# Kernel optimization log

Measured on AMD Instinct MI355X. Metric: run time of the kernel, lower is better.

## Reference

```python
import jax, jax.numpy as jnp
import numpy as np

B, S, D, H = 2, 2048, 1024, 16
DK = D // H


def setup_inputs() -> dict:
    key = jax.random.key(0)
    ks = jax.random.split(key, 12)
    sc = 1.0 / np.sqrt(D)
    inp = {
        'q': jax.random.normal(ks[0], (B, S, D), jnp.float32),
        'k': jax.random.normal(ks[1], (B, S, D), jnp.float32),
        'v': jax.random.normal(ks[2], (B, S, D), jnp.float32),
        'mask': jnp.tril(jnp.ones((S, S), jnp.int32))[None, None],  # causal [1,1,S,S]
        'w_q': jax.random.normal(ks[3], (D, D), jnp.float32) * sc,
        'b_q': jnp.zeros((D,), jnp.float32),
        'w_k': jax.random.normal(ks[4], (D, D), jnp.float32) * sc,
        'b_k': jnp.zeros((D,), jnp.float32),
        'w_v': jax.random.normal(ks[5], (D, D), jnp.float32) * sc,
        'b_v': jnp.zeros((D,), jnp.float32),
        'w_o': jax.random.normal(ks[6], (D, D), jnp.float32) * sc,
        'b_o': jnp.zeros((D,), jnp.float32),
    }
    return inp


def _split_heads(x):
    # [B,S,D] -> [B,H,S,DK]
    b, s, _ = x.shape
    return x.reshape(b, s, H, DK).transpose(0, 2, 1, 3)


def reference(q, k, v, mask, w_q, b_q, w_k, b_k, w_v, b_v, w_o, b_o):
    # Linear projections (torch Linear: x @ W.T + b)
    qh = _split_heads(q @ w_q.T + b_q)
    kh = _split_heads(k @ w_k.T + b_k)
    vh = _split_heads(v @ w_v.T + b_v)
    scores = jnp.einsum('bhqd,bhkd->bhqk', qh, kh) / jnp.sqrt(jnp.float32(DK))
    scores = jnp.where(mask == 0, jnp.float32(-1e9), scores)
    probs = jax.nn.softmax(scores, axis=-1)
    # dropout is identity in eval mode
    ctx = jnp.einsum('bhqk,bhkd->bhqd', probs, vh)  # [B,H,S,DK]
    ctx = ctx.transpose(0, 2, 1, 3).reshape(q.shape[0], -1, D)
    out = ctx @ w_o.T + b_o
    return out, probs
```

## Files before the change

kernel.cpp:

```cpp
#include <hip/hip_runtime.h>

typedef float f32x4 __attribute__((ext_vector_type(4)));
typedef short s16x8 __attribute__((ext_vector_type(8)));
typedef short s16x4 __attribute__((ext_vector_type(4)));

#define MFMA(a, b, c) __builtin_amdgcn_mfma_f32_16x16x32_bf16((a), (b), (c), 0, 0, 0)

static __device__ __forceinline__ short f2bf(float f) {
  union { float ff; unsigned u; } v; v.ff = f;
  unsigned r = v.u + 0x7FFFu + ((v.u >> 16) & 1u);
  return (short)(r >> 16);
}
static __device__ __forceinline__ float bf2f(short s) {
  union { unsigned u; float f; } v;
  v.u = ((unsigned)(unsigned short)s) << 16;
  return v.f;
}

typedef __attribute__((address_space(3))) void lds_void_t;
typedef const __attribute__((address_space(1))) void gmem_void_t;
static __device__ __forceinline__ void gload_lds16(const void* g, void* l) {
  __builtin_amdgcn_global_load_lds((gmem_void_t*)g, (lds_void_t*)l, 16, 0, 0);
}

__global__ __launch_bounds__(256) void cvt_qkv_kernel(
    const float* __restrict__ q, const float* __restrict__ k, const float* __restrict__ v,
    short* __restrict__ qo, short* __restrict__ ko, short* __restrict__ vo) {
  const int y = blockIdx.y;
  const float* s = (y == 0) ? q : (y == 1) ? k : v;
  short* d = (y == 0) ? qo : (y == 1) ? ko : vo;
  const int i = blockIdx.x * 256 + threadIdx.x;
  const f32x4* s4 = (const f32x4*)s;
  f32x4 a = s4[2 * i], b = s4[2 * i + 1];
  s16x8 o;
  o[0] = f2bf(a[0]); o[1] = f2bf(a[1]); o[2] = f2bf(a[2]); o[3] = f2bf(a[3]);
  o[4] = f2bf(b[0]); o[5] = f2bf(b[1]); o[6] = f2bf(b[2]); o[7] = f2bf(b[3]);
  ((s16x8*)d)[i] = o;
}

__global__ __launch_bounds__(256) void cvt_w_kernel(
    const float* __restrict__ w0, const float* __restrict__ w1,
    const float* __restrict__ w2, const float* __restrict__ w3,
    short* __restrict__ o0, short* __restrict__ o1,
    short* __restrict__ o2, short* __restrict__ o3) {
  const int y = blockIdx.y;
  const float* s = (y == 0) ? w0 : (y == 1) ? w1 : (y == 2) ? w2 : w3;
  short* d = (y == 0) ? o0 : (y == 1) ? o1 : (y == 2) ? o2 : o3;
  const int i = blockIdx.x * 256 + threadIdx.x;
  const f32x4* s4 = (const f32x4*)s;
  f32x4 a = s4[2 * i], b = s4[2 * i + 1];
  s16x8 o;
  o[0] = f2bf(a[0]); o[1] = f2bf(a[1]); o[2] = f2bf(a[2]); o[3] = f2bf(a[3]);
  o[4] = f2bf(b[0]); o[5] = f2bf(b[1]); o[6] = f2bf(b[2]); o[7] = f2bf(b[3]);
  ((s16x8*)d)[i] = o;
}

template <int MODE, int NFRAG>
static __device__ __forceinline__ void gemm_body(
    const short* __restrict__ A, const short* __restrict__ Bt,
    const float* __restrict__ bias, void* __restrict__ outp) {
  constexpr int BN = NFRAG * 32;
  __shared__ short As[4096];
  __shared__ short Bs[BN * 32];
  const int t = threadIdx.x;
  const int lane = t & 63, wave = t >> 6;
  const int wr = wave >> 1, wc = wave & 1;
  const int lr = lane & 15, lg = lane >> 4;
  const int mBase = blockIdx.x * 128, nBase = blockIdx.y * BN;

  const int rowA = t >> 2, kcA = (t & 3) << 3;
  const short* gA = A + (size_t)(mBase + rowA) * 1024 + kcA;
  const short* gB = Bt + (size_t)(nBase + rowA) * 1024 + kcA;

  f32x4 acc[4][NFRAG] = {};

  for (int k0 = 0; k0 < 1024; k0 += 32) {
    __syncthreads();
    gload_lds16(gA + k0, &As[t * 8]);
    gload_lds16(gA + 64 * 1024 + k0, &As[2048 + t * 8]);
    gload_lds16(gB + k0, &Bs[t * 8]);
    if constexpr (NFRAG == 4) gload_lds16(gB + 64 * 1024 + k0, &Bs[2048 + t * 8]);
    __syncthreads();
    const s16x8* Av = (const s16x8*)As;
    const s16x8* Bv = (const s16x8*)Bs;
    s16x8 af[4], bfr[NFRAG];
#pragma unroll
    for (int m = 0; m < 4; ++m) af[m] = Av[(wr * 64 + m * 16 + lr) * 4 + lg];
#pragma unroll
    for (int n = 0; n < NFRAG; ++n) bfr[n] = Bv[(wc * NFRAG * 16 + n * 16 + lr) * 4 + lg];
#pragma unroll
    for (int m = 0; m < 4; ++m)
#pragma unroll
      for (int n = 0; n < NFRAG; ++n)
        acc[m][n] = MFMA(af[m], bfr[n], acc[m][n]);
  }

  const int row0 = mBase + wr * 64 + lg * 4;
  const int col0 = nBase + wc * NFRAG * 16 + lr;
#pragma unroll
  for (int n = 0; n < NFRAG; ++n) {
    const int col = col0 + n * 16;
    const float bv = bias[col];
#pragma unroll
    for (int m = 0; m < 4; ++m) {
#pragma unroll
      for (int j = 0; j < 4; ++j) {
        const int r = row0 + m * 16 + j;
        const float val = acc[m][n][j] + bv;
        if (MODE == 0) {
          short* o = (short*)outp;
          const int bb = r >> 11, ss = r & 2047, hh = col >> 6, dd = col & 63;
          o[((size_t)(bb * 16 + hh) * 2048 + ss) * 64 + dd] = f2bf(val);
        } else {
          ((float*)outp)[(size_t)r * 1024 + col] = val;
        }
      }
    }
  }
}

__global__ __launch_bounds__(256) void gemm_qkv_kernel(
    const short* __restrict__ qb, const short* __restrict__ kb, const short* __restrict__ vb,
    const short* __restrict__ wqb, const short* __restrict__ wkb, const short* __restrict__ wvb,
    const float* __restrict__ bq, const float* __restrict__ bk, const float* __restrict__ bv,
    short* __restrict__ Qh, short* __restrict__ Kh, short* __restrict__ Vh) {
  const int z = blockIdx.z;
  const short* A  = (z == 0) ? qb : (z == 1) ? kb : vb;
  const short* Bt = (z == 0) ? wqb : (z == 1) ? wkb : wvb;
  const float* bias = (z == 0) ? bq : (z == 1) ? bk : bv;
  short* out = (z == 0) ? Qh : (z == 1) ? Kh : Vh;
  gemm_body<0, 4>(A, Bt, bias, out);
}

__global__ __launch_bounds__(256) void gemm_o_kernel(
    const short* __restrict__ A, const short* __restrict__ Bt,
    const float* __restrict__ bias, float* __restrict__ outp) {
  gemm_body<1, 2>(A, Bt, bias, outp);
}

__global__ __launch_bounds__(256) void attn_kernel(
    const short* __restrict__ Qh, const short* __restrict__ Kh,
    const short* __restrict__ Vh, float* __restrict__ probs,
    short* __restrict__ ctxo) {
  __shared__ short Ks[2][4096];
  __shared__ short Vt[2][4096];
  __shared__ short Pl[4096];
  const int t = threadIdx.x;
  const int lane = t & 63, w = t >> 6;
  const int lr = lane & 15, lg = lane >> 4;
  const int qblk = 31 - blockIdx.x;
  const int bh = blockIdx.y;
  const size_t hb = (size_t)bh * (2048 * 64);
  const int qBase = qblk * 64;

  const short* Kg = Kh + hb;
  const short* Vg = Vh + hb;

  const int qg = qBase + w * 16 + lr;
  const s16x8 qf0 = *(const s16x8*)(Qh + hb + (size_t)qg * 64 + lg * 8);
  const s16x8 qf1 = *(const s16x8*)(Qh + hb + (size_t)qg * 64 + 32 + lg * 8);

  const int x = lr & 7;
  const int px = (lr & 7) << 3;

  {
    const f32x4 zz = {0.f, 0.f, 0.f, 0.f};
#pragma unroll 1
    for (int r = 0; r < 16; ++r) {
      float* prow = probs + (size_t)(bh * 2048 + qBase + w * 16 + r) * 2048;
      for (int c = qBase + 64 + lane * 4; c < 2048; c += 256)
        *(f32x4*)&prow[c] = zz;
    }
  }

  auto stageK = [&](int buf, int kt) {
    const int kBase = kt * 64;
    int c = t, key = c >> 3, slot = c & 7;
    gload_lds16(Kg + (size_t)(kBase + key) * 64 + ((slot ^ (key & 7)) << 3), &Ks[buf][c * 8]);
    c = t + 256; key = c >> 3; slot = c & 7;
    gload_lds16(Kg + (size_t)(kBase + key) * 64 + ((slot ^ (key & 7)) << 3), &Ks[buf][c * 8]);
  };

  float rs = 0.f;
  stageK(0, 0);
  __syncthreads();
  for (int kt = 0; kt <= qblk; ++kt) {
    const int cur = kt & 1;
    if (kt < qblk) stageK(cur ^ 1, kt + 1);
    const s16x8* Kv = (const s16x8*)Ks[cur];
#pragma unroll
    for (int sub = 0; sub < 4; ++sub) {
      const int key = sub * 16 + lr;
      s16x8 kf0 = Kv[key * 8 + (lg ^ x)];
      s16x8 kf1 = Kv[key * 8 + ((lg + 4) ^ x)];
      f32x4 z = {0.f, 0.f, 0.f, 0.f};
      f32x4 sa = MFMA(kf0, qf0, z);
      sa = MFMA(kf1, qf1, sa);
      if (kt < qblk) {
#pragma unroll
        for (int j = 0; j < 4; ++j) rs += __expf(sa[j] * 0.125f);
      } else {
        const int key0 = kt * 64 + sub * 16 + lg * 4;
#pragma unroll
        for (int j = 0; j < 4; ++j)
          if (key0 + j <= qg) rs += __expf(sa[j] * 0.125f);
      }
    }
    __syncthreads();
  }
  rs += __shfl_xor(rs, 16);
  rs += __shfl_xor(rs, 32);
  const float rinv = 1.f / rs;

  const int vkey = lane, vdkb = w * 16;
  auto loadV = [&](int kt, s16x8& v0, s16x8& v1) {
    const s16x8* vsrc = (const s16x8*)(Vg + (size_t)(kt * 64 + vkey) * 64 + vdkb);
    v0 = vsrc[0]; v1 = vsrc[1];
  };
  auto writeV = [&](int buf, const s16x8& v0, const s16x8& v1) {
#pragma unroll
    for (int i = 0; i < 8; ++i) {
      const int r0 = vdkb + i, r1 = vdkb + 8 + i;
      Vt[buf][r0 * 64 + (vkey ^ ((r0 & 7) << 3))] = v0[i];
      Vt[buf][r1 * 64 + (vkey ^ ((r1 & 7) << 3))] = v1[i];
    }
  };

  f32x4 cacc[4] = {};
  {
    s16x8 v0, v1;
    stageK(0, 0);
    loadV(0, v0, v1);
    writeV(0, v0, v1);
    __syncthreads();
  }
  for (int kt = 0; kt <= qblk; ++kt) {
    const int cur = kt & 1;
    const bool pf = (kt < qblk);
    const int kBase = kt * 64;
    s16x8 nv0, nv1;
    if (pf) { stageK(cur ^ 1, kt + 1); loadV(kt + 1, nv0, nv1); }
    const s16x8* Kv = (const s16x8*)Ks[cur];
#pragma unroll
    for (int sub = 0; sub < 4; ++sub) {
      const int key = sub * 16 + lr;
      s16x8 kf0 = Kv[key * 8 + (lg ^ x)];
      s16x8 kf1 = Kv[key * 8 + ((lg + 4) ^ x)];
      f32x4 z = {0.f, 0.f, 0.f, 0.f};
      f32x4 sa = MFMA(kf0, qf0, z);
      sa = MFMA(kf1, qf1, sa);
      const int key0 = kBase + sub * 16 + lg * 4;
      f32x4 p4;
      if (kt < qblk) {
#pragma unroll
        for (int j = 0; j < 4; ++j) p4[j] = __expf(sa[j] * 0.125f) * rinv;
      } else {
#pragma unroll
        for (int j = 0; j < 4; ++j)
          p4[j] = (key0 + j <= qg) ? __expf(sa[j] * 0.125f) * rinv : 0.f;
      }
      s16x4 pb;
      pb[0] = f2bf(p4[0]); pb[1] = f2bf(p4[1]);
      pb[2] = f2bf(p4[2]); pb[3] = f2bf(p4[3]);
      *(s16x4*)&Pl[w * 1024 + lr * 64 + ((sub * 16 + lg * 4) ^ px)] = pb;
    }
#pragma unroll
    for (int it = 0; it < 4; ++it) {
      const int row = it * 4 + lg;
      const int c = lr * 4;
      const s16x4 pb4 = *(const s16x4*)&Pl[w * 1024 + row * 64 + (c ^ ((row & 7) << 3))];
      f32x4 pf4;
      pf4[0] = bf2f(pb4[0]); pf4[1] = bf2f(pb4[1]);
      pf4[2] = bf2f(pb4[2]); pf4[3] = bf2f(pb4[3]);
      *(f32x4*)&probs[(size_t)(bh * 2048 + qBase + w * 16 + row) * 2048 + kBase + c] = pf4;
    }
    if (pf) writeV(cur ^ 1, nv0, nv1);
    const s16x8* Vv = (const s16x8*)Vt[cur];
    const s16x8 pfa = *(const s16x8*)&Pl[w * 1024 + lr * 64 + ((lg * 8) ^ px)];
    const s16x8 pfb = *(const s16x8*)&Pl[w * 1024 + lr * 64 + ((32 + lg * 8) ^ px)];
#pragma unroll
    for (int n = 0; n < 4; ++n) {
      const int row = n * 16 + lr;
      s16x8 vf0 = Vv[row * 8 + (lg ^ x)];
      s16x8 vf1 = Vv[row * 8 + ((lg + 4) ^ x)];
      cacc[n] = MFMA(pfa, vf0, cacc[n]);
      cacc[n] = MFMA(pfb, vf1, cacc[n]);
    }
    __syncthreads();
  }

  const int bb = bh >> 4, hh = bh & 15;
#pragma unroll
  for (int n = 0; n < 4; ++n) {
    const int dcol = hh * 64 + n * 16 + lr;
#pragma unroll
    for (int j = 0; j < 4; ++j) {
      const int srow = qBase + w * 16 + lg * 4 + j;
      ctxo[(size_t)(bb * 2048 + srow) * 1024 + dcol] = f2bf(cacc[n][j]);
    }
  }
}

extern "C" void kernel_launch(void* const* d_in, const int* in_sizes, int n_in,
                              void* d_out, int out_size, void* d_ws, size_t ws_size,
                              hipStream_t stream) {
  const float* q  = (const float*)d_in[0];
  const float* k  = (const float*)d_in[1];
  const float* v  = (const float*)d_in[2];
  const float* wq = (const float*)d_in[4];
  const float* bq = (const float*)d_in[5];
  const float* wk = (const float*)d_in[6];
  const float* bk = (const float*)d_in[7];
  const float* wv = (const float*)d_in[8];
  const float* bv = (const float*)d_in[9];
  const float* wo = (const float*)d_in[10];
  const float* bo = (const float*)d_in[11];

  char* ws = (char*)d_ws;
  const size_t MB = 1u << 20;
  short* qb  = (short*)(ws);
  short* kb  = (short*)(ws + 8 * MB);
  short* vb  = (short*)(ws + 16 * MB);
  short* wqb = (short*)(ws + 24 * MB);
  short* wkb = (short*)(ws + 26 * MB);
  short* wvb = (short*)(ws + 28 * MB);
  short* wob = (short*)(ws + 30 * MB);
  short* Qh  = (short*)(ws + 32 * MB);
  short* Kh  = (short*)(ws + 40 * MB);
  short* Vh  = (short*)(ws + 48 * MB);
  short* ctx = (short*)(ws + 56 * MB);

  float* outp  = (float*)d_out;
  float* probs = outp + (size_t)4096 * 1024;

  cvt_qkv_kernel<<<dim3(2048, 3), 256, 0, stream>>>(q, k, v, qb, kb, vb);
  cvt_w_kernel<<<dim3(512, 4), 256, 0, stream>>>(wq, wk, wv, wo, wqb, wkb, wvb, wob);

  gemm_qkv_kernel<<<dim3(32, 8, 3), 256, 0, stream>>>(
      qb, kb, vb, wqb, wkb, wvb, bq, bk, bv, Qh, Kh, Vh);

  attn_kernel<<<dim3(32, 32), 256, 0, stream>>>(Qh, Kh, Vh, probs, ctx);

  gemm_o_kernel<<<dim3(32, 16), 256, 0, stream>>>(ctx, wob, bo, outp);
}
```

Measured before the change: 750.4 us.

## Split softmax row-sum pass into separate kernel and read K directly from global

Moves the first attention pass, which computes softmax denominators, into its own rowsum_kernel that writes reciprocal row sums to workspace (reusing the qb region, which is dead by then). The attention kernel reads those values instead of recomputing them. Both kernels now load K fragments straight from global memory instead of staging them through double-buffered LDS with async copies. This drops LDS use and barriers and may raise occupancy, at the cost of an extra launch and uncoalesced, repeated global K reads that rely on cache.

Result: slower. 914.8 us (+21.9%).

```diff
diff --git a/kernel.cpp b/kernel.cpp
--- a/kernel.cpp
+++ b/kernel.cpp
@@ -138,11 +138,53 @@
   gemm_body<1, 2>(A, Bt, bias, outp);
 }
 
+__global__ __launch_bounds__(256) void rowsum_kernel(
+    const short* __restrict__ Qh, const short* __restrict__ Kh,
+    float* __restrict__ rinv) {
+  const int t = threadIdx.x;
+  const int lane = t & 63, w = t >> 6;
+  const int lr = lane & 15, lg = lane >> 4;
+  const int qblk = 31 - blockIdx.x;
+  const int bh = blockIdx.y;
+  const size_t hb = (size_t)bh * (2048 * 64);
+  const int qBase = qblk * 64;
+  const int qg = qBase + w * 16 + lr;
+
+  const s16x8 qf0 = *(const s16x8*)(Qh + hb + (size_t)qg * 64 + lg * 8);
+  const s16x8 qf1 = *(const s16x8*)(Qh + hb + (size_t)qg * 64 + 32 + lg * 8);
+  const short* Kg = Kh + hb;
+
+  float rs = 0.f;
+  for (int kt = 0; kt <= qblk; ++kt) {
+    const int kBase = kt * 64;
+#pragma unroll
+    for (int sub = 0; sub < 4; ++sub) {
+      const int key = kBase + sub * 16 + lr;
+      const s16x8 kf0 = *(const s16x8*)(Kg + (size_t)key * 64 + lg * 8);
+      const s16x8 kf1 = *(const s16x8*)(Kg + (size_t)key * 64 + 32 + lg * 8);
+      f32x4 z = {0.f, 0.f, 0.f, 0.f};
+      f32x4 sa = MFMA(kf0, qf0, z);
+      sa = MFMA(kf1, qf1, sa);
+      if (kt < qblk) {
+#pragma unroll
+        for (int j = 0; j < 4; ++j) rs += __expf(sa[j] * 0.125f);
+      } else {
+        const int key0 = kBase + sub * 16 + lg * 4;
+#pragma unroll
+        for (int j = 0; j < 4; ++j)
+          if (key0 + j <= qg) rs += __expf(sa[j] * 0.125f);
+      }
+    }
+  }
+  rs += __shfl_xor(rs, 16);
+  rs += __shfl_xor(rs, 32);
+  if (lg == 0) rinv[bh * 2048 + qg] = 1.f / rs;
+}
+
 __global__ __launch_bounds__(256) void attn_kernel(
     const short* __restrict__ Qh, const short* __restrict__ Kh,
-    const short* __restrict__ Vh, float* __restrict__ probs,
-    short* __restrict__ ctxo) {
-  __shared__ short Ks[2][4096];
+    const short* __restrict__ Vh, const float* __restrict__ rinv_g,
+    float* __restrict__ probs, short* __restrict__ ctxo) {
   __shared__ short Vt[2][4096];
   __shared__ short Pl[4096];
   const int t = threadIdx.x;
@@ -159,6 +201,7 @@
   const int qg = qBase + w * 16 + lr;
   const s16x8 qf0 = *(const s16x8*)(Qh + hb + (size_t)qg * 64 + lg * 8);
   const s16x8 qf1 = *(const s16x8*)(Qh + hb + (size_t)qg * 64 + 32 + lg * 8);
+  const float rinv = rinv_g[bh * 2048 + qg];
 
   const int x = lr & 7;
   const int px = (lr & 7) << 3;
@@ -173,45 +216,6 @@
     }
   }
 
-  auto stageK = [&](int buf, int kt) {
-    const int kBase = kt * 64;
-    int c = t, key = c >> 3, slot = c & 7;
-    gload_lds16(Kg + (size_t)(kBase + key) * 64 + ((slot ^ (key & 7)) << 3), &Ks[buf][c * 8]);
-    c = t + 256; key = c >> 3; slot = c & 7;
-    gload_lds16(Kg + (size_t)(kBase + key) * 64 + ((slot ^ (key & 7)) << 3), &Ks[buf][c * 8]);
-  };
-
-  float rs = 0.f;
-  stageK(0, 0);
-  __syncthreads();
-  for (int kt = 0; kt <= qblk; ++kt) {
-    const int cur = kt & 1;
-    if (kt < qblk) stageK(cur ^ 1, kt + 1);
-    const s16x8* Kv = (const s16x8*)Ks[cur];
-#pragma unroll
-    for (int sub = 0; sub < 4; ++sub) {
-      const int key = sub * 16 + lr;
-      s16x8 kf0 = Kv[key * 8 + (lg ^ x)];
-      s16x8 kf1 = Kv[key * 8 + ((lg + 4) ^ x)];
-      f32x4 z = {0.f, 0.f, 0.f, 0.f};
-      f32x4 sa = MFMA(kf0, qf0, z);
-      sa = MFMA(kf1, qf1, sa);
-      if (kt < qblk) {
-#pragma unroll
-        for (int j = 0; j < 4; ++j) rs += __expf(sa[j] * 0.125f);
-      } else {
-        const int key0 = kt * 64 + sub * 16 + lg * 4;
-#pragma unroll
-        for (int j = 0; j < 4; ++j)
-          if (key0 + j <= qg) rs += __expf(sa[j] * 0.125f);
-      }
-    }
-    __syncthreads();
-  }
-  rs += __shfl_xor(rs, 16);
-  rs += __shfl_xor(rs, 32);
-  const float rinv = 1.f / rs;
-
   const int vkey = lane, vdkb = w * 16;
   auto loadV = [&](int kt, s16x8& v0, s16x8& v1) {
     const s16x8* vsrc = (const s16x8*)(Vg + (size_t)(kt * 64 + vkey) * 64 + vdkb);
@@ -229,7 +233,6 @@
   f32x4 cacc[4] = {};
   {
     s16x8 v0, v1;
-    stageK(0, 0);
     loadV(0, v0, v1);
     writeV(0, v0, v1);
     __syncthreads();
@@ -239,13 +242,12 @@
     const bool pf = (kt < qblk);
     const int kBase = kt * 64;
     s16x8 nv0, nv1;
-    if (pf) { stageK(cur ^ 1, kt + 1); loadV(kt + 1, nv0, nv1); }
-    const s16x8* Kv = (const s16x8*)Ks[cur];
+    if (pf) loadV(kt + 1, nv0, nv1);
 #pragma unroll
     for (int sub = 0; sub < 4; ++sub) {
-      const int key = sub * 16 + lr;
-      s16x8 kf0 = Kv[key * 8 + (lg ^ x)];
-      s16x8 kf1 = Kv[key * 8 + ((lg + 4) ^ x)];
+      const int key = kBase + sub * 16 + lr;
+      const s16x8 kf0 = *(const s16x8*)(Kg + (size_t)key * 64 + lg * 8);
+      const s16x8 kf1 = *(const s16x8*)(Kg + (size_t)key * 64 + 32 + lg * 8);
       f32x4 z = {0.f, 0.f, 0.f, 0.f};
       f32x4 sa = MFMA(kf0, qf0, z);
       sa = MFMA(kf1, qf1, sa);
@@ -329,6 +331,7 @@
   short* Kh  = (short*)(ws + 40 * MB);
   short* Vh  = (short*)(ws + 48 * MB);
   short* ctx = (short*)(ws + 56 * MB);
+  float* rinv = (float*)(ws);
 
   float* outp  = (float*)d_out;
   float* probs = outp + (size_t)4096 * 1024;
@@ -339,7 +342,9 @@
   gemm_qkv_kernel<<<dim3(32, 8, 3), 256, 0, stream>>>(
       qb, kb, vb, wqb, wkb, wvb, bq, bk, bv, Qh, Kh, Vh);
 
-  attn_kernel<<<dim3(32, 32), 256, 0, stream>>>(Qh, Kh, Vh, probs, ctx);
+  rowsum_kernel<<<dim3(32, 32), 256, 0, stream>>>(Qh, Kh, rinv);
+
+  attn_kernel<<<dim3(32, 32), 256, 0, stream>>>(Qh, Kh, Vh, rinv, probs, ctx);
 
   gemm_o_kernel<<<dim3(32, 16), 256, 0, stream>>>(ctx, wob, bo, outp);
 }
```

## Pre-transpose V in a separate kernel and load V fragments directly from global

Applied to the files above, without the earlier changes.

Adds a kernel that writes V transposed per head into workspace, so the attention kernel can load MFMA B-operand fragments for P·V straight from global memory. This drops the LDS double buffer for V and its scalar transposing writes, which cuts LDS use, and launch_bounds now asks for 4 blocks per multiprocessor. In exchange it adds an extra kernel launch and a global round trip for V. The V loads now sit on the critical path each iteration instead of being prefetched into LDS. An unused pointer argument is added to the attention kernel.

Result: slower. 811.5 us (+8.2%).

```diff
diff --git a/kernel.cpp b/kernel.cpp
--- a/kernel.cpp
+++ b/kernel.cpp
@@ -138,12 +138,30 @@
   gemm_body<1, 2>(A, Bt, bias, outp);
 }
 
-__global__ __launch_bounds__(256) void attn_kernel(
+__global__ __launch_bounds__(256) void vtrans_kernel(
+    const short* __restrict__ Vh, short* __restrict__ Vt_g) {
+  const int kBase = blockIdx.x * 64;
+  const int bh = blockIdx.y;
+  const size_t ib = (size_t)bh * (2048 * 64);
+  const size_t ob = (size_t)bh * (64 * 2048);
+  const int t = threadIdx.x;
+  const int dk = t >> 2, k8 = t & 3;
+#pragma unroll
+  for (int h = 0; h < 2; ++h) {
+    const int kk = (k8 + 4 * h) * 8;
+    s16x8 v;
+#pragma unroll
+    for (int j = 0; j < 8; ++j)
+      v[j] = Vh[ib + (size_t)(kBase + kk + j) * 64 + dk];
+    *(s16x8*)&Vt_g[ob + (size_t)dk * 2048 + kBase + kk] = v;
+  }
+}
+
+__global__ __launch_bounds__(256, 4) void attn_kernel(
     const short* __restrict__ Qh, const short* __restrict__ Kh,
-    const short* __restrict__ Vh, float* __restrict__ probs,
-    short* __restrict__ ctxo) {
+    const short* __restrict__ Vt_g, const float* __restrict__ rinv_unused,
+    float* __restrict__ probs, short* __restrict__ ctxo) {
   __shared__ short Ks[2][4096];
-  __shared__ short Vt[2][4096];
   __shared__ short Pl[4096];
   const int t = threadIdx.x;
   const int lane = t & 63, w = t >> 6;
@@ -154,7 +172,7 @@
   const int qBase = qblk * 64;
 
   const short* Kg = Kh + hb;
-  const short* Vg = Vh + hb;
+  const short* Vth = Vt_g + (size_t)bh * (64 * 2048);
 
   const int qg = qBase + w * 16 + lr;
   const s16x8 qf0 = *(const s16x8*)(Qh + hb + (size_t)qg * 64 + lg * 8);
@@ -212,34 +230,13 @@
   rs += __shfl_xor(rs, 32);
   const float rinv = 1.f / rs;
 
-  const int vkey = lane, vdkb = w * 16;
-  auto loadV = [&](int kt, s16x8& v0, s16x8& v1) {
-    const s16x8* vsrc = (const s16x8*)(Vg + (size_t)(kt * 64 + vkey) * 64 + vdkb);
-    v0 = vsrc[0]; v1 = vsrc[1];
-  };
-  auto writeV = [&](int buf, const s16x8& v0, const s16x8& v1) {
-#pragma unroll
-    for (int i = 0; i < 8; ++i) {
-      const int r0 = vdkb + i, r1 = vdkb + 8 + i;
-      Vt[buf][r0 * 64 + (vkey ^ ((r0 & 7) << 3))] = v0[i];
-      Vt[buf][r1 * 64 + (vkey ^ ((r1 & 7) << 3))] = v1[i];
-    }
-  };
-
   f32x4 cacc[4] = {};
-  {
-    s16x8 v0, v1;
-    stageK(0, 0);
-    loadV(0, v0, v1);
-    writeV(0, v0, v1);
-    __syncthreads();
-  }
+  stageK(0, 0);
+  __syncthreads();
   for (int kt = 0; kt <= qblk; ++kt) {
     const int cur = kt & 1;
-    const bool pf = (kt < qblk);
     const int kBase = kt * 64;
-    s16x8 nv0, nv1;
-    if (pf) { stageK(cur ^ 1, kt + 1); loadV(kt + 1, nv0, nv1); }
+    if (kt < qblk) stageK(cur ^ 1, kt + 1);
     const s16x8* Kv = (const s16x8*)Ks[cur];
 #pragma unroll
     for (int sub = 0; sub < 4; ++sub) {
@@ -264,6 +261,13 @@
       pb[2] = f2bf(p4[2]); pb[3] = f2bf(p4[3]);
       *(s16x4*)&Pl[w * 1024 + lr * 64 + ((sub * 16 + lg * 4) ^ px)] = pb;
     }
+    s16x8 vf0[4], vf1[4];
+#pragma unroll
+    for (int n = 0; n < 4; ++n) {
+      const short* vrow = Vth + (size_t)(n * 16 + lr) * 2048 + kBase + lg * 8;
+      vf0[n] = *(const s16x8*)vrow;
+      vf1[n] = *(const s16x8*)(vrow + 32);
+    }
 #pragma unroll
     for (int it = 0; it < 4; ++it) {
       const int row = it * 4 + lg;
@@ -274,17 +278,12 @@
       pf4[2] = bf2f(pb4[2]); pf4[3] = bf2f(pb4[3]);
       *(f32x4*)&probs[(size_t)(bh * 2048 + qBase + w * 16 + row) * 2048 + kBase + c] = pf4;
     }
-    if (pf) writeV(cur ^ 1, nv0, nv1);
-    const s16x8* Vv = (const s16x8*)Vt[cur];
     const s16x8 pfa = *(const s16x8*)&Pl[w * 1024 + lr * 64 + ((lg * 8) ^ px)];
     const s16x8 pfb = *(const s16x8*)&Pl[w * 1024 + lr * 64 + ((32 + lg * 8) ^ px)];
 #pragma unroll
     for (int n = 0; n < 4; ++n) {
-      const int row = n * 16 + lr;
-      s16x8 vf0 = Vv[row * 8 + (lg ^ x)];
-      s16x8 vf1 = Vv[row * 8 + ((lg + 4) ^ x)];
-      cacc[n] = MFMA(pfa, vf0, cacc[n]);
-      cacc[n] = MFMA(pfb, vf1, cacc[n]);
+      cacc[n] = MFMA(pfa, vf0[n], cacc[n]);
+      cacc[n] = MFMA(pfb, vf1[n], cacc[n]);
     }
     __syncthreads();
   }
@@ -329,6 +328,7 @@
   short* Kh  = (short*)(ws + 40 * MB);
   short* Vh  = (short*)(ws + 48 * MB);
   short* ctx = (short*)(ws + 56 * MB);
+  short* Vtg = (short*)(ws + 64 * MB);
 
   float* outp  = (float*)d_out;
   float* probs = outp + (size_t)4096 * 1024;
@@ -339,7 +339,9 @@
   gemm_qkv_kernel<<<dim3(32, 8, 3), 256, 0, stream>>>(
       qb, kb, vb, wqb, wkb, wvb, bq, bk, bv, Qh, Kh, Vh);
 
-  attn_kernel<<<dim3(32, 32), 256, 0, stream>>>(Qh, Kh, Vh, probs, ctx);
+  vtrans_kernel<<<dim3(32, 32), 256, 0, stream>>>(Vh, Vtg);
+
+  attn_kernel<<<dim3(32, 32), 256, 0, stream>>>(Qh, Kh, Vtg, nullptr, probs, ctx);
 
   gemm_o_kernel<<<dim3(32, 16), 256, 0, stream>>>(ctx, wob, bo, outp);
 }
```
